# Performance work log

Measured on AMD Instinct MI355X. Metric: run time of the kernel, lower is better.

Reference implementation:

```python
import jax, jax.numpy as jnp
import numpy as np

N_NODES = 100000
N_EDGES = 1600000
F_IN = 128
F_OUT = 64


def setup_inputs() -> dict:
    key = jax.random.key(0)
    k0, k1, k2, k3, k4, k5 = jax.random.split(key, 6)
    stdv = 1.0 / np.sqrt(F_OUT)
    x = jax.random.normal(k0, (N_NODES, F_IN), dtype=jnp.float32)
    edge_src = jax.random.randint(k1, (N_EDGES,), 0, N_NODES, dtype=jnp.int32)
    edge_dst = jax.random.randint(k2, (N_EDGES,), 0, N_NODES, dtype=jnp.int32)
    # normalized adjacency values (all positive, like D^-1/2 A D^-1/2 entries)
    edge_weight = jax.random.uniform(k3, (N_EDGES,), dtype=jnp.float32)
    weight = jax.random.uniform(k4, (F_IN, F_OUT), dtype=jnp.float32, minval=-stdv, maxval=stdv)
    bias = jax.random.uniform(k5, (F_OUT,), dtype=jnp.float32, minval=-stdv, maxval=stdv)
    return {"x": x, "edge_weight": edge_weight, "weight": weight, "bias": bias,
            "edge_src": edge_src, "edge_dst": edge_dst}


def reference(x, edge_weight, weight, bias, edge_src, edge_dst):
    # support = X @ W  -- dense GEMM [N, F_in] x [F_in, F_out]
    support = x @ weight
    # spmm(adj, support): adj in COO form; gather source rows, scale by edge value,
    # scatter-add into destination rows.
    msgs = support[edge_src] * edge_weight[:, None]          # [E, F_out]
    out = jax.ops.segment_sum(msgs, edge_dst, num_segments=x.shape[0])
    return out + bias
```

## Files before the change

kernel.cpp:

```cpp
#include <hip/hip_runtime.h>
#include <hip/hip_bf16.h>

#define F_IN 128
#define F_OUT 64
#define BUCKET_SHIFT 7
#define BUCKET_NODES 128
#define BUCKET_CAP 2880
#define CNT_STRIDE 16
#define NB_MAX 800
#define SCAT_CHUNK 8192
#define EPT 8
#define P1_GEMM_ROWS 128
#define LDK 136
#define SA_EPT 3

typedef __attribute__((ext_vector_type(8))) short bf16x8;
typedef __attribute__((ext_vector_type(4))) float f32x4;

__device__ inline short bf16_bits(float f) {
  __hip_bfloat16 h = __float2bfloat16(f);
  return *reinterpret_cast<short*>(&h);
}

union Phase1Smem {
  struct { short Bs[F_OUT][LDK]; } g;
  struct { int lhist[NB_MAX]; int lcur[NB_MAX]; } s;
};

__global__ __launch_bounds__(1024, 2) void gcn_phase1_kernel(
    const float* __restrict__ x, const float* __restrict__ w,
    __hip_bfloat16* __restrict__ support,
    const int* __restrict__ esrc, const int* __restrict__ edst,
    const float* __restrict__ ew, int* __restrict__ bcount,
    int2* __restrict__ region, int n_nodes, int n_edges, int nb,
    int n_scat_blocks) {
  __shared__ Phase1Smem sm;
  const int tid = threadIdx.x;

  if ((int)blockIdx.x < n_scat_blocks) {
    const int e0 = blockIdx.x * SCAT_CHUNK;
    const int n_local = min(SCAT_CHUNK, n_edges - e0);

    for (int i = tid; i < nb; i += 1024) sm.s.lhist[i] = 0;
    __syncthreads();
    int dreg[EPT];
#pragma unroll
    for (int p = 0; p < EPT; ++p) {
      const int i = tid + p * 1024;
      dreg[p] = -1;
      if (i < n_local) {
        const int d = edst[e0 + i];
        dreg[p] = d;
        atomicAdd(&sm.s.lhist[d >> BUCKET_SHIFT], 1);
      }
    }
    __syncthreads();
    for (int b = tid; b < nb; b += 1024) {
      const int c = sm.s.lhist[b];
      sm.s.lcur[b] = c ? atomicAdd(&bcount[b * CNT_STRIDE], c) : 0;
    }
    __syncthreads();
#pragma unroll
    for (int p = 0; p < EPT; ++p) {
      const int i = tid + p * 1024;
      const int d = dreg[p];
      if (d >= 0) {
        const int b = d >> BUCKET_SHIFT;
        const int pos = atomicAdd(&sm.s.lcur[b], 1);
        if (pos < BUCKET_CAP) {
          region[(size_t)b * BUCKET_CAP + pos] = make_int2(
              (esrc[e0 + i] << BUCKET_SHIFT) | (d & (BUCKET_NODES - 1)),
              __float_as_int(ew[e0 + i]));
        }
      }
    }
  } else {
    const int gbid = (int)blockIdx.x - n_scat_blocks;
    const int block_row = gbid * P1_GEMM_ROWS;

#pragma unroll
    for (int i = 0; i < F_IN * F_OUT / 1024; ++i) {
      const int idx = tid + i * 1024;
      sm.g.Bs[idx & 63][idx >> 6] = bf16_bits(w[idx]);
    }

    const int lane = tid & 63;
    const int wid = tid >> 6;
    const int wr0 = (wid >> 1) * 16;
    const int wc0 = (wid & 1) * 32;
    const int m = lane & 15;
    const int quad = lane >> 4;
    const int row = block_row + wr0 + m;

    bf16x8 afrag[4];
    if (row < n_nodes) {
      const float4* xr = (const float4*)(x + (size_t)row * F_IN);
#pragma unroll
      for (int ks = 0; ks < 4; ++ks) {
        const float4 v0 = xr[ks * 8 + quad * 2];
        const float4 v1 = xr[ks * 8 + quad * 2 + 1];
        bf16x8 a;
        a[0] = bf16_bits(v0.x); a[1] = bf16_bits(v0.y);
        a[2] = bf16_bits(v0.z); a[3] = bf16_bits(v0.w);
        a[4] = bf16_bits(v1.x); a[5] = bf16_bits(v1.y);
        a[6] = bf16_bits(v1.z); a[7] = bf16_bits(v1.w);
        afrag[ks] = a;
      }
    } else {
#pragma unroll
      for (int ks = 0; ks < 4; ++ks) afrag[ks] = (bf16x8)0;
    }
    __syncthreads();

    f32x4 acc0 = {0.f, 0.f, 0.f, 0.f};
    f32x4 acc1 = {0.f, 0.f, 0.f, 0.f};
#pragma unroll
    for (int ks = 0; ks < 4; ++ks) {
      const int ko = ks * 32 + quad * 8;
      const bf16x8 b0 = *(const bf16x8*)&sm.g.Bs[wc0 + m][ko];
      const bf16x8 b1 = *(const bf16x8*)&sm.g.Bs[wc0 + 16 + m][ko];
      acc0 = __builtin_amdgcn_mfma_f32_16x16x32_bf16(afrag[ks], b0, acc0, 0, 0, 0);
      acc1 = __builtin_amdgcn_mfma_f32_16x16x32_bf16(afrag[ks], b1, acc1, 0, 0, 0);
    }
#pragma unroll
    for (int r = 0; r < 4; ++r) {
      const int orow = block_row + wr0 + quad * 4 + r;
      if (orow < n_nodes) {
        __hip_bfloat16* op = support + (size_t)orow * F_OUT;
        op[wc0 + m]      = __float2bfloat16(acc0[r]);
        op[wc0 + 16 + m] = __float2bfloat16(acc1[r]);
      }
    }
  }
}

__global__ __launch_bounds__(1024, 2) void gcn_sort_agg_kernel(
    const __hip_bfloat16* __restrict__ support,
    const int2* __restrict__ region, const int* __restrict__ bcount,
    const float* __restrict__ bias, float* __restrict__ out, int n_nodes) {
  __shared__ int2 outb[BUCKET_CAP];
  __shared__ int hist4[4][BUCKET_NODES];
  __shared__ int nbeg[BUCKET_NODES];
  __shared__ int lcur[BUCKET_NODES];
  const int b = blockIdx.x;
  const int tid = threadIdx.x;
  const int lane = tid & 63;
  const int hq = (tid >> 6) & 3;

  int cnt = bcount[b * CNT_STRIDE];
  cnt = (cnt < BUCKET_CAP ? cnt : BUCKET_CAP);
  const int2* reg = region + (size_t)b * BUCKET_CAP;

  for (int i = tid; i < 4 * BUCKET_NODES; i += 1024) ((int*)hist4)[i] = 0;
  __syncthreads();
  int2 ereg[SA_EPT];
#pragma unroll
  for (int p = 0; p < SA_EPT; ++p) {
    const int i = tid + p * 1024;
    ereg[p].x = -1;
    if (i < cnt) {
      ereg[p] = reg[i];
      atomicAdd(&hist4[hq][ereg[p].x & (BUCKET_NODES - 1)], 1);
    }
  }
  __syncthreads();
  if (tid < 64) {
    const int v0 = hist4[0][lane] + hist4[1][lane] + hist4[2][lane] +
                   hist4[3][lane];
    const int l1 = 64 + lane;
    const int v1 = hist4[0][l1] + hist4[1][l1] + hist4[2][l1] + hist4[3][l1];
    int s0 = v0;
#pragma unroll
    for (int off = 1; off < 64; off <<= 1) {
      const int t = __shfl_up(s0, off, 64);
      if (lane >= off) s0 += t;
    }
    const int tot0 = __shfl(s0, 63, 64);
    int s1 = v1;
#pragma unroll
    for (int off = 1; off < 64; off <<= 1) {
      const int t = __shfl_up(s1, off, 64);
      if (lane >= off) s1 += t;
    }
    s1 += tot0;
    nbeg[lane] = s0 - v0;
    nbeg[l1] = s1 - v1;
    lcur[lane] = s0 - v0;
    lcur[l1] = s1 - v1;
  }
  __syncthreads();
#pragma unroll
  for (int p = 0; p < SA_EPT; ++p) {
    if (ereg[p].x >= 0) {
      const int pos = atomicAdd(&lcur[ereg[p].x & (BUCKET_NODES - 1)], 1);
      outb[pos] = make_int2(ereg[p].x >> BUCKET_SHIFT, ereg[p].y);
    }
  }
  __syncthreads();

  const int wid = tid >> 6;
  const int r = lane >> 3;
  const int cg = lane & 7;
  const ushort* sup = (const ushort*)support;
  const float4 bb0 = *(const float4*)(bias + cg * 8);
  const float4 bb1 = *(const float4*)(bias + cg * 8 + 4);
  for (int nl = wid * 8; nl < wid * 8 + 8; ++nl) {
    const int g = (b << BUCKET_SHIFT) + nl;
    if (g >= n_nodes) break;
    const int s = nbeg[nl];
    const int e = lcur[nl];
    float acc[8] = {0.f, 0.f, 0.f, 0.f, 0.f, 0.f, 0.f, 0.f};
    for (int j = s; j < e; j += 8) {
      const int jr = j + r;
      const bool valid = jr < e;
      const int2 meta = outb[valid ? jr : e - 1];
      const float wv = valid ? __int_as_float(meta.y) : 0.f;
      const uint4 d = *(const uint4*)(sup + (size_t)meta.x * F_OUT + cg * 8);
      acc[0] = fmaf(__uint_as_float(d.x << 16), wv, acc[0]);
      acc[1] = fmaf(__uint_as_float(d.x & 0xffff0000u), wv, acc[1]);
      acc[2] = fmaf(__uint_as_float(d.y << 16), wv, acc[2]);
      acc[3] = fmaf(__uint_as_float(d.y & 0xffff0000u), wv, acc[3]);
      acc[4] = fmaf(__uint_as_float(d.z << 16), wv, acc[4]);
      acc[5] = fmaf(__uint_as_float(d.z & 0xffff0000u), wv, acc[5]);
      acc[6] = fmaf(__uint_as_float(d.w << 16), wv, acc[6]);
      acc[7] = fmaf(__uint_as_float(d.w & 0xffff0000u), wv, acc[7]);
    }
#pragma unroll
    for (int i = 0; i < 8; ++i) {
      float v = acc[i];
      v += __shfl_xor(v, 8, 64);
      v += __shfl_xor(v, 16, 64);
      v += __shfl_xor(v, 32, 64);
      acc[i] = v;
    }
    if (r == 0) {
      float* op = out + (size_t)g * F_OUT + cg * 8;
      float4 o0, o1;
      o0.x = acc[0] + bb0.x; o0.y = acc[1] + bb0.y;
      o0.z = acc[2] + bb0.z; o0.w = acc[3] + bb0.w;
      o1.x = acc[4] + bb1.x; o1.y = acc[5] + bb1.y;
      o1.z = acc[6] + bb1.z; o1.w = acc[7] + bb1.w;
      *(float4*)op = o0;
      *(float4*)(op + 4) = o1;
    }
  }
}

extern "C" void kernel_launch(void* const* d_in, const int* in_sizes, int n_in,
                              void* d_out, int out_size, void* d_ws, size_t ws_size,
                              hipStream_t stream) {
  const float* x    = (const float*)d_in[0];
  const float* ew   = (const float*)d_in[1];
  const float* w    = (const float*)d_in[2];
  const float* bias = (const float*)d_in[3];
  const int*   esrc = (const int*)d_in[4];
  const int*   edst = (const int*)d_in[5];
  float* out = (float*)d_out;

  const int n_nodes = in_sizes[0] / F_IN;
  const int n_edges = in_sizes[4];
  const int nb = (n_nodes + BUCKET_NODES - 1) >> BUCKET_SHIFT;

  char* ws = (char*)d_ws;
  size_t off = 0;
  auto alloc = [&](size_t bytes) {
    size_t o = off;
    off += (bytes + 255) / 256 * 256;
    return o;
  };
  const size_t off_bcount  = alloc((size_t)nb * CNT_STRIDE * sizeof(int));
  const size_t off_region  = alloc((size_t)nb * BUCKET_CAP * sizeof(int2));
  const size_t off_support = alloc((size_t)n_nodes * F_OUT * sizeof(__hip_bfloat16));
  (void)off_support;

  int*  bcount = (int*)(ws + off_bcount);
  int2* region = (int2*)(ws + off_region);
  __hip_bfloat16* support = (__hip_bfloat16*)(ws + off_support);

  const int scat_blocks = (n_edges + SCAT_CHUNK - 1) / SCAT_CHUNK;
  const int gemm_blocks = (n_nodes + P1_GEMM_ROWS - 1) / P1_GEMM_ROWS;

  hipMemsetAsync(bcount, 0, (size_t)nb * CNT_STRIDE * sizeof(int), stream);
  gcn_phase1_kernel<<<scat_blocks + gemm_blocks, 1024, 0, stream>>>(
      x, w, support, esrc, edst, ew, bcount, region, n_nodes, n_edges, nb,
      scat_blocks);
  gcn_sort_agg_kernel<<<nb, 1024, 0, stream>>>(support, region, bcount, bias,
                                               out, n_nodes);
}
```

Measured before the change: 196.5 us.

## Pad bucket slots to multiples of eight, double scatter chunk, unroll gather loop

Scatter blocks now reserve bucket space in multiples of eight and fill the unused slots with zero-weight dummy edges. Each scatter block handles twice as many edges, and the min-blocks-per-SM launch bound is dropped. The aggregation loop processes sixteen edges per iteration with two independent accumulators to keep more gather loads in flight. Padding raises bucket counts, which the sort kernel presumably has to handle; those lines are not visible, and the padding eats into BUCKET_CAP headroom, so overflow truncation becomes more likely.

```diff
diff --git a/kernel.cpp b/kernel.cpp
--- a/kernel.cpp
+++ b/kernel.cpp
@@ -8,8 +8,8 @@
 #define BUCKET_CAP 2880
 #define CNT_STRIDE 16
 #define NB_MAX 800
-#define SCAT_CHUNK 8192
-#define EPT 8
+#define SCAT_CHUNK 16384
+#define EPT 16
 #define P1_GEMM_ROWS 128
 #define LDK 136
 #define SA_EPT 3
@@ -27,7 +27,7 @@
   struct { int lhist[NB_MAX]; int lcur[NB_MAX]; } s;
 };
 
-__global__ __launch_bounds__(1024, 2) void gcn_phase1_kernel(
+__global__ __launch_bounds__(1024) void gcn_phase1_kernel(
     const float* __restrict__ x, const float* __restrict__ w,
     __hip_bfloat16* __restrict__ support,
     const int* __restrict__ esrc, const int* __restrict__ edst,
@@ -57,7 +57,8 @@
     __syncthreads();
     for (int b = tid; b < nb; b += 1024) {
       const int c = sm.s.lhist[b];
-      sm.s.lcur[b] = c ? atomicAdd(&bcount[b * CNT_STRIDE], c) : 0;
+      const int rc = (c + 7) & ~7;
+      sm.s.lcur[b] = rc ? atomicAdd(&bcount[b * CNT_STRIDE], rc) : 0;
     }
     __syncthreads();
 #pragma unroll
@@ -74,6 +75,18 @@
         }
       }
     }
+    __syncthreads();
+    for (int b = tid; b < nb; b += 1024) {
+      const int c = sm.s.lhist[b];
+      const int npad = (8 - (c & 7)) & 7;
+      const int start = sm.s.lcur[b];
+      for (int k = 0; k < npad; ++k) {
+        const int pos = start + k;
+        if (pos < BUCKET_CAP)
+          region[(size_t)b * BUCKET_CAP + pos] =
+              make_int2(pos & (BUCKET_NODES - 1), 0);
+      }
+    }
   } else {
     const int gbid = (int)blockIdx.x - n_scat_blocks;
     const int block_row = gbid * P1_GEMM_ROWS;
@@ -134,7 +147,7 @@
   }
 }
 
-__global__ __launch_bounds__(1024, 2) void gcn_sort_agg_kernel(
+__global__ __launch_bounds__(1024) void gcn_sort_agg_kernel(
     const __hip_bfloat16* __restrict__ support,
     const int2* __restrict__ region, const int* __restrict__ bcount,
     const float* __restrict__ bias, float* __restrict__ out, int n_nodes) {
@@ -209,37 +222,51 @@
     if (g >= n_nodes) break;
     const int s = nbeg[nl];
     const int e = lcur[nl];
-    float acc[8] = {0.f, 0.f, 0.f, 0.f, 0.f, 0.f, 0.f, 0.f};
-    for (int j = s; j < e; j += 8) {
-      const int jr = j + r;
-      const bool valid = jr < e;
-      const int2 meta = outb[valid ? jr : e - 1];
-      const float wv = valid ? __int_as_float(meta.y) : 0.f;
-      const uint4 d = *(const uint4*)(sup + (size_t)meta.x * F_OUT + cg * 8);
-      acc[0] = fmaf(__uint_as_float(d.x << 16), wv, acc[0]);
-      acc[1] = fmaf(__uint_as_float(d.x & 0xffff0000u), wv, acc[1]);
-      acc[2] = fmaf(__uint_as_float(d.y << 16), wv, acc[2]);
-      acc[3] = fmaf(__uint_as_float(d.y & 0xffff0000u), wv, acc[3]);
-      acc[4] = fmaf(__uint_as_float(d.z << 16), wv, acc[4]);
-      acc[5] = fmaf(__uint_as_float(d.z & 0xffff0000u), wv, acc[5]);
-      acc[6] = fmaf(__uint_as_float(d.w << 16), wv, acc[6]);
-      acc[7] = fmaf(__uint_as_float(d.w & 0xffff0000u), wv, acc[7]);
+    float acc0[8] = {0.f, 0.f, 0.f, 0.f, 0.f, 0.f, 0.f, 0.f};
+    float acc1[8] = {0.f, 0.f, 0.f, 0.f, 0.f, 0.f, 0.f, 0.f};
+    for (int j = s; j < e; j += 16) {
+      const int jr0 = j + r;
+      const int jr1 = j + 8 + r;
+      const bool v0 = jr0 < e;
+      const bool v1 = jr1 < e;
+      const int2 m0 = outb[v0 ? jr0 : s];
+      const int2 m1 = outb[v1 ? jr1 : s];
+      const float w0 = v0 ? __int_as_float(m0.y) : 0.f;
+      const float w1 = v1 ? __int_as_float(m1.y) : 0.f;
+      const uint4 d0 = *(const uint4*)(sup + (size_t)m0.x * F_OUT + cg * 8);
+      const uint4 d1 = *(const uint4*)(sup + (size_t)m1.x * F_OUT + cg * 8);
+      acc0[0] = fmaf(__uint_as_float(d0.x << 16), w0, acc0[0]);
+      acc0[1] = fmaf(__uint_as_float(d0.x & 0xffff0000u), w0, acc0[1]);
+      acc0[2] = fmaf(__uint_as_float(d0.y << 16), w0, acc0[2]);
+      acc0[3] = fmaf(__uint_as_float(d0.y & 0xffff0000u), w0, acc0[3]);
+      acc0[4] = fmaf(__uint_as_float(d0.z << 16), w0, acc0[4]);
+      acc0[5] = fmaf(__uint_as_float(d0.z & 0xffff0000u), w0, acc0[5]);
+      acc0[6] = fmaf(__uint_as_float(d0.w << 16), w0, acc0[6]);
+      acc0[7] = fmaf(__uint_as_float(d0.w & 0xffff0000u), w0, acc0[7]);
+      acc1[0] = fmaf(__uint_as_float(d1.x << 16), w1, acc1[0]);
+      acc1[1] = fmaf(__uint_as_float(d1.x & 0xffff0000u), w1, acc1[1]);
+      acc1[2] = fmaf(__uint_as_float(d1.y << 16), w1, acc1[2]);
+      acc1[3] = fmaf(__uint_as_float(d1.y & 0xffff0000u), w1, acc1[3]);
+      acc1[4] = fmaf(__uint_as_float(d1.z << 16), w1, acc1[4]);
+      acc1[5] = fmaf(__uint_as_float(d1.z & 0xffff0000u), w1, acc1[5]);
+      acc1[6] = fmaf(__uint_as_float(d1.w << 16), w1, acc1[6]);
+      acc1[7] = fmaf(__uint_as_float(d1.w & 0xffff0000u), w1, acc1[7]);
     }
 #pragma unroll
     for (int i = 0; i < 8; ++i) {
-      float v = acc[i];
+      float v = acc0[i] + acc1[i];
       v += __shfl_xor(v, 8, 64);
       v += __shfl_xor(v, 16, 64);
       v += __shfl_xor(v, 32, 64);
-      acc[i] = v;
+      acc0[i] = v;
     }
     if (r == 0) {
       float* op = out + (size_t)g * F_OUT + cg * 8;
       float4 o0, o1;
-      o0.x = acc[0] + bb0.x; o0.y = acc[1] + bb0.y;
-      o0.z = acc[2] + bb0.z; o0.w = acc[3] + bb0.w;
-      o1.x = acc[4] + bb1.x; o1.y = acc[5] + bb1.y;
-      o1.z = acc[6] + bb1.z; o1.w = acc[7] + bb1.w;
+      o0.x = acc0[0] + bb0.x; o0.y = acc0[1] + bb0.y;
+      o0.z = acc0[2] + bb0.z; o0.w = acc0[3] + bb0.w;
+      o1.x = acc0[4] + bb1.x; o1.y = acc0[5] + bb1.y;
+      o1.z = acc0[6] + bb1.z; o1.w = acc0[7] + bb1.w;
       *(float4*)op = o0;
       *(float4*)(op + 4) = o1;
     }
```

New measurement: 194.9 us. About the same (-0.8%).
